# Optimization experiments

Measured on AMD Instinct MI355X. Metric: run time of the kernel, lower is better.

## Reference

```python
import jax, jax.numpy as jnp
import numpy as np

N, M, D = 16384, 1024, 1024


def setup_inputs() -> dict:
    key = jax.random.key(0)
    kq, kp = jax.random.split(key)
    query = jax.random.normal(kq, (N, D), dtype=jnp.float32)
    proto = jax.random.normal(kp, (M, D), dtype=jnp.float32)
    return {"query": query, "proto": proto}


def reference(query, proto):
    # Pairwise squared euclidean: ||q||^2 - 2 q.p + ||p||^2  (same math as
    # the expand+pow+sum in compute_euclidean, but without the [N,M,D] blowup).
    q2 = jnp.sum(query * query, axis=-1, keepdims=True)          # [N,1]
    p2 = jnp.sum(proto * proto, axis=-1)                          # [M]
    qp = jnp.einsum('nd,md->nm', query, proto)                    # [N,M]
    dists = q2 - 2.0 * qp + p2[None, :]                           # [N,M]
    # Original applies F.softmax(-dists, dim=1) (named log_p_y but is softmax).
    return jax.nn.softmax(-dists, axis=1)
```

## Files before the change

kernel.cpp:

```cpp
#include <hip/hip_runtime.h>
#include <stdint.h>

#define N_Q 16384
#define M_P 1024
#define D_K 1024

typedef __attribute__((ext_vector_type(8))) __bf16 bf16x8;
typedef __attribute__((ext_vector_type(4))) float floatx4;
typedef __attribute__((ext_vector_type(4))) unsigned int uint4v;

#define AS1 __attribute__((address_space(1)))
#define AS3 __attribute__((address_space(3)))

__device__ __forceinline__ unsigned short f2bf(float f) {
    unsigned int u = __float_as_uint(f);
    u += 0x7fffu + ((u >> 16) & 1u);
    return (unsigned short)(u >> 16);
}
__device__ __forceinline__ float bf2f(unsigned short h) {
    return __uint_as_float(((unsigned int)h) << 16);
}

__device__ __forceinline__ void split_chunk(floatx4 f0, floatx4 f1,
                                            uint4v* hi, uint4v* lo) {
    float e[8] = {f0.x, f0.y, f0.z, f0.w, f1.x, f1.y, f1.z, f1.w};
    unsigned int hb[4], lb[4];
#pragma unroll
    for (int p = 0; p < 4; ++p) {
        unsigned int u0 = __float_as_uint(e[2 * p]);
        unsigned int u1 = __float_as_uint(e[2 * p + 1]);
        hb[p] = __builtin_amdgcn_perm(u1, u0, 0x07060302);
        float l0 = e[2 * p]     - __uint_as_float(u0 & 0xffff0000u);
        float l1 = e[2 * p + 1] - __uint_as_float(u1 & 0xffff0000u);
        lb[p] = __builtin_amdgcn_perm(__float_as_uint(l1), __float_as_uint(l0),
                                      0x07060302);
    }
    uint4v h = {hb[0], hb[1], hb[2], hb[3]};
    uint4v l = {lb[0], lb[1], lb[2], lb[3]};
    *hi = h;
    *lo = l;
}

__global__ __launch_bounds__(256) void convert_proto_kernel(
    const float* __restrict__ proto, unsigned short* __restrict__ ph,
    unsigned short* __restrict__ pl, float* __restrict__ p2) {
    __shared__ float sred[4];
    int m = blockIdx.x;
    int t = threadIdx.x;
    size_t base4 = (size_t)m * (D_K / 4) + t;
    float4 v = ((const float4*)proto)[base4];
    ushort4 h, l;
    h.x = f2bf(v.x); l.x = f2bf(v.x - bf2f(h.x));
    h.y = f2bf(v.y); l.y = f2bf(v.y - bf2f(h.y));
    h.z = f2bf(v.z); l.z = f2bf(v.z - bf2f(h.z));
    h.w = f2bf(v.w); l.w = f2bf(v.w - bf2f(h.w));
    ((ushort4*)ph)[base4] = h;
    ((ushort4*)pl)[base4] = l;
    float sq = v.x * v.x + v.y * v.y + v.z * v.z + v.w * v.w;
#pragma unroll
    for (int off = 1; off < 64; off <<= 1) sq += __shfl_xor(sq, off);
    if ((t & 63) == 0) sred[t >> 6] = sq;
    __syncthreads();
    if (t == 0) p2[m] = sred[0] + sred[1] + sred[2] + sred[3];
}

__global__ __launch_bounds__(512, 2) void gemm_logits_kernel(
    const float* __restrict__ query,
    const unsigned short* __restrict__ ph, const unsigned short* __restrict__ pl,
    const float* __restrict__ p2, float* __restrict__ out) {
    __shared__ unsigned short sAh[2][16 * 512];
    __shared__ unsigned short sAl[2][16 * 512];
    __shared__ unsigned short sBh[2][16 * 512];
    __shared__ unsigned short sBl[2][16 * 512];

    const int tid = threadIdx.x;
    const int wave = tid >> 6;
    const int lane = tid & 63;
    const int wr = wave >> 2;
    const int wc = wave & 3;

    const int b = blockIdx.x;
    const int v = (b & 7) * 32 + (b >> 3);
    const int colt = v >> 6;
    const int rowt = v & 63;
    const int row0 = rowt * 256;
    const int col0 = colt * 256;

    const int rlB = lane >> 2;
    const int cioB = (lane & 3) ^ ((lane >> 3) & 3);
    const int halfB = wave >> 2;
    const int sgB = wave & 3;
    const unsigned short* gB = (halfB ? pl : ph)
        + (size_t)(col0 + sgB * 64 + rlB) * D_K + cioB * 8;

    const int rlA = lane >> 2;
    const int cA = lane & 3;
    const float* gA = query + (size_t)(row0 + wave * 32 + rlA) * D_K + cA * 8;
    const int wroff = (4 * rlA + (cA ^ ((rlA >> 1) & 3))) * 8;

    const int rsel = lane & 15;
    const int kq = lane >> 4;
    const int fragoff = (4 * rsel + (kq ^ ((rsel >> 1) & 3))) * 8;

    floatx4 zero = {0.0f, 0.0f, 0.0f, 0.0f};
    floatx4 acc[8][4];
#pragma unroll
    for (int i = 0; i < 8; ++i)
#pragma unroll
        for (int j = 0; j < 4; ++j) acc[i][j] = zero;

    floatx4 f0[2], f1[2];
    bf16x8 bh[4], bl[4];
    bf16x8 ah[2], al[2];

    auto issueA = [&](int kb) {
#pragma unroll
        for (int s = 0; s < 2; ++s) {
            const float* p = gA + (size_t)(s * 16) * D_K + kb;
            f0[s] = *(const floatx4*)p;
            f1[s] = *(const floatx4*)(p + 4);
        }
    };
    auto issueB = [&](int kb, int nxt) {
        unsigned short* dstB = (halfB ? sBl[nxt] : sBh[nxt]) + sgB * 4 * 512;
#pragma unroll
        for (int s = 0; s < 4; ++s)
            __builtin_amdgcn_global_load_lds(
                (const AS1 unsigned int*)(const void*)(gB + (size_t)(s * 16) * D_K + kb),
                (AS3 unsigned int*)(void*)(dstB + s * 512), 16, 0, 0);
    };
    auto writeA = [&](int nxt, int s) {
        uint4v hi, lo;
        split_chunk(f0[s], f1[s], &hi, &lo);
        const int off = (wave * 2 + s) * 512 + wroff;
        *(uint4v*)(sAh[nxt] + off) = hi;
        *(uint4v*)(sAl[nxt] + off) = lo;
    };
    auto ldBfrag = [&](int cur) {
#pragma unroll
        for (int j = 0; j < 4; ++j) {
            const int boff = (wc * 4 + j) * 512 + fragoff;
            bh[j] = *(const bf16x8*)(sBh[cur] + boff);
            bl[j] = *(const bf16x8*)(sBl[cur] + boff);
        }
    };
    auto ldAfrag = [&](int cur, int i0) {
#pragma unroll
        for (int t = 0; t < 2; ++t) {
            const int aoff = (wr * 8 + i0 + t) * 512 + fragoff;
            ah[t] = *(const bf16x8*)(sAh[cur] + aoff);
            al[t] = *(const bf16x8*)(sAl[cur] + aoff);
        }
    };
    auto mfma2 = [&](int i0) {
#pragma unroll
        for (int j = 0; j < 4; ++j)
#pragma unroll
            for (int t = 0; t < 2; ++t) {
                acc[i0 + t][j] = __builtin_amdgcn_mfma_f32_16x16x32_bf16(ah[t], bh[j], acc[i0 + t][j], 0, 0, 0);
                acc[i0 + t][j] = __builtin_amdgcn_mfma_f32_16x16x32_bf16(ah[t], bl[j], acc[i0 + t][j], 0, 0, 0);
                acc[i0 + t][j] = __builtin_amdgcn_mfma_f32_16x16x32_bf16(al[t], bh[j], acc[i0 + t][j], 0, 0, 0);
            }
    };

    auto stepf = [&](int kbn, int cur, int nxt, bool pf) {
        if (pf) { issueA(kbn); issueB(kbn, nxt); }
        ldBfrag(cur);
        ldAfrag(cur, 0);
        __builtin_amdgcn_s_barrier();
        __builtin_amdgcn_s_setprio(1); mfma2(0); __builtin_amdgcn_s_setprio(0);
        __builtin_amdgcn_s_barrier();
        ldAfrag(cur, 2);
        __builtin_amdgcn_s_barrier();
        __builtin_amdgcn_s_setprio(1); mfma2(2); __builtin_amdgcn_s_setprio(0);
        __builtin_amdgcn_s_barrier();
        ldAfrag(cur, 4);
        if (pf) writeA(nxt, 0);
        __builtin_amdgcn_s_barrier();
        __builtin_amdgcn_s_setprio(1); mfma2(4); __builtin_amdgcn_s_setprio(0);
        __builtin_amdgcn_s_barrier();
        ldAfrag(cur, 6);
        if (pf) writeA(nxt, 1);
        __syncthreads();
        __builtin_amdgcn_s_setprio(1); mfma2(6); __builtin_amdgcn_s_setprio(0);
    };

    issueA(0);
    issueB(0, 0);
    writeA(0, 0);
    writeA(0, 1);
    __syncthreads();

    for (int kt = 0; kt < 30; kt += 2) {
        stepf((kt + 1) * 32, 0, 1, true);
        stepf((kt + 2) * 32, 1, 0, true);
    }
    stepf(31 * 32, 0, 1, true);
    stepf(0, 1, 0, false);

#pragma unroll
    for (int j = 0; j < 4; ++j) {
        const int gc = col0 + wc * 64 + j * 16 + rsel;
        const float p2v = p2[gc];
#pragma unroll
        for (int i = 0; i < 8; ++i) {
            const int gr = row0 + wr * 128 + i * 16 + kq * 4;
#pragma unroll
            for (int r = 0; r < 4; ++r) {
                out[(size_t)(gr + r) * M_P + gc] = 2.0f * acc[i][j][r] - p2v;
            }
        }
    }
}

__global__ __launch_bounds__(256) void naive_logits_kernel(
    const float* __restrict__ query, const float* __restrict__ proto,
    float* __restrict__ out) {
    __shared__ float qs[D_K];
    int n = blockIdx.x;
    int t = threadIdx.x;
    ((float4*)qs)[t] = ((const float4*)(query + (size_t)n * D_K))[t];
    __syncthreads();
    float acc[4] = {0.f, 0.f, 0.f, 0.f};
    float pp[4] = {0.f, 0.f, 0.f, 0.f};
    for (int d = 0; d < D_K; d += 4) {
        float4 qv = *(const float4*)(qs + d);
#pragma unroll
        for (int j = 0; j < 4; ++j) {
            const float4 pv = *(const float4*)(proto + (size_t)(t + 256 * j) * D_K + d);
            acc[j] += qv.x * pv.x + qv.y * pv.y + qv.z * pv.z + qv.w * pv.w;
            pp[j] += pv.x * pv.x + pv.y * pv.y + pv.z * pv.z + pv.w * pv.w;
        }
    }
#pragma unroll
    for (int j = 0; j < 4; ++j)
        out[(size_t)n * M_P + t + 256 * j] = 2.0f * acc[j] - pp[j];
}

__global__ __launch_bounds__(256) void softmax_kernel(float* __restrict__ out) {
    const int lane = threadIdx.x & 63;
    int n = blockIdx.x * 4 + (threadIdx.x >> 6);
    for (int it = 0; it < 2; ++it, n += 8192) {
        float* row = out + (size_t)n * M_P;
        floatx4 v[4];
#pragma unroll
        for (int k = 0; k < 4; ++k)
            v[k] = *((const floatx4*)row + k * 64 + lane);
        float mx = fmaxf(fmaxf(v[0].x, v[0].y), fmaxf(v[0].z, v[0].w));
#pragma unroll
        for (int k = 1; k < 4; ++k)
            mx = fmaxf(mx, fmaxf(fmaxf(v[k].x, v[k].y), fmaxf(v[k].z, v[k].w)));
#pragma unroll
        for (int off = 1; off < 64; off <<= 1) mx = fmaxf(mx, __shfl_xor(mx, off));
        float s = 0.0f;
#pragma unroll
        for (int k = 0; k < 4; ++k) {
            v[k].x = __expf(v[k].x - mx);
            v[k].y = __expf(v[k].y - mx);
            v[k].z = __expf(v[k].z - mx);
            v[k].w = __expf(v[k].w - mx);
            s += v[k].x + v[k].y + v[k].z + v[k].w;
        }
#pragma unroll
        for (int off = 1; off < 64; off <<= 1) s += __shfl_xor(s, off);
        const float inv = 1.0f / s;
#pragma unroll
        for (int k = 0; k < 4; ++k) {
            floatx4 o;
            o.x = v[k].x * inv; o.y = v[k].y * inv;
            o.z = v[k].z * inv; o.w = v[k].w * inv;
            __builtin_nontemporal_store(o, (floatx4*)row + k * 64 + lane);
        }
    }
}

extern "C" void kernel_launch(void* const* d_in, const int* in_sizes, int n_in,
                              void* d_out, int out_size, void* d_ws, size_t ws_size,
                              hipStream_t stream) {
    const float* query = (const float*)d_in[0];
    const float* proto = (const float*)d_in[1];
    float* out = (float*)d_out;

    const size_t pElems = (size_t)M_P * D_K;
    const size_t needed = pElems * 2 * 2 + M_P * 4;

    if (ws_size >= needed) {
        unsigned short* ph = (unsigned short*)d_ws;
        unsigned short* pl = ph + pElems;
        float* p2 = (float*)(pl + pElems);

        convert_proto_kernel<<<M_P, 256, 0, stream>>>(proto, ph, pl, p2);
        gemm_logits_kernel<<<(N_Q / 256) * (M_P / 256), 512, 0, stream>>>(
            query, ph, pl, p2, out);
    } else {
        naive_logits_kernel<<<N_Q, 256, 0, stream>>>(query, proto, out);
    }
    softmax_kernel<<<2048, 256, 0, stream>>>(out);
}
```

Baseline: 206.6 us.

## Prefetch query tile one step further ahead with explicit waitcnt scheduling

The query (A) global loads are issued one k-step earlier, so the register-held fp32 data for step k+2 is in flight while step k computes, and both A-chunk writes to LDS move to the middle phase. Manual s_waitcnt lgkmcnt/vmcnt plus sched_barrier replace __syncthreads, so the wait is only on the B async LDS loads and the A loads stay outstanding. The A pointer is cast to global address space so the compiler emits global rather than flat loads. This adds register pressure and relies on exact vmcnt counts, which must match the number of outstanding loads.

```diff
diff --git a/kernel.cpp b/kernel.cpp
--- a/kernel.cpp
+++ b/kernel.cpp
@@ -95,7 +95,8 @@
 
     const int rlA = lane >> 2;
     const int cA = lane & 3;
-    const float* gA = query + (size_t)(row0 + wave * 32 + rlA) * D_K + cA * 8;
+    const AS1 float* gA = (const AS1 float*)query
+        + (size_t)(row0 + wave * 32 + rlA) * D_K + cA * 8;
     const int wroff = (4 * rlA + (cA ^ ((rlA >> 1) & 3))) * 8;
 
     const int rsel = lane & 15;
@@ -116,9 +117,9 @@
     auto issueA = [&](int kb) {
 #pragma unroll
         for (int s = 0; s < 2; ++s) {
-            const float* p = gA + (size_t)(s * 16) * D_K + kb;
-            f0[s] = *(const floatx4*)p;
-            f1[s] = *(const floatx4*)(p + 4);
+            const AS1 float* p = gA + (size_t)(s * 16) * D_K + kb;
+            f0[s] = *(const AS1 floatx4*)p;
+            f1[s] = *(const AS1 floatx4*)(p + 4);
         }
     };
     auto issueB = [&](int kb, int nxt) {
@@ -163,40 +164,56 @@
             }
     };
 
-    auto stepf = [&](int kbn, int cur, int nxt, bool pf) {
-        if (pf) { issueA(kbn); issueB(kbn, nxt); }
+#define PHASE_MFMA(i0)                                          \
+    __builtin_amdgcn_s_barrier();                               \
+    asm volatile("s_waitcnt lgkmcnt(0)" ::: "memory");          \
+    __builtin_amdgcn_sched_barrier(0);                          \
+    __builtin_amdgcn_s_setprio(1);                              \
+    mfma2(i0);                                                  \
+    __builtin_amdgcn_s_setprio(0);                              \
+    __builtin_amdgcn_s_barrier();
+
+    auto stepf = [&](int kbnB, int kbnA, int cur, int nxt, bool pfB, bool pfA) {
+        if (pfB) issueB(kbnB, nxt);
         ldBfrag(cur);
         ldAfrag(cur, 0);
+        PHASE_MFMA(0)
+        ldAfrag(cur, 2);
+        PHASE_MFMA(2)
+        ldAfrag(cur, 4);
+        if (pfB) { writeA(nxt, 0); writeA(nxt, 1); }
+        PHASE_MFMA(4)
+        ldAfrag(cur, 6);
+        if (pfA) issueA(kbnA);
+        asm volatile("s_waitcnt lgkmcnt(0)" ::: "memory");
+        if (pfB) {
+            if (pfA) asm volatile("s_waitcnt vmcnt(4)" ::: "memory");
+            else     asm volatile("s_waitcnt vmcnt(0)" ::: "memory");
+        }
         __builtin_amdgcn_s_barrier();
-        __builtin_amdgcn_s_setprio(1); mfma2(0); __builtin_amdgcn_s_setprio(0);
-        __builtin_amdgcn_s_barrier();
-        ldAfrag(cur, 2);
-        __builtin_amdgcn_s_barrier();
-        __builtin_amdgcn_s_setprio(1); mfma2(2); __builtin_amdgcn_s_setprio(0);
-        __builtin_amdgcn_s_barrier();
-        ldAfrag(cur, 4);
-        if (pf) writeA(nxt, 0);
-        __builtin_amdgcn_s_barrier();
-        __builtin_amdgcn_s_setprio(1); mfma2(4); __builtin_amdgcn_s_setprio(0);
-        __builtin_amdgcn_s_barrier();
-        ldAfrag(cur, 6);
-        if (pf) writeA(nxt, 1);
-        __syncthreads();
-        __builtin_amdgcn_s_setprio(1); mfma2(6); __builtin_amdgcn_s_setprio(0);
+        __builtin_amdgcn_sched_barrier(0);
+        __builtin_amdgcn_s_setprio(1);
+        mfma2(6);
+        __builtin_amdgcn_s_setprio(0);
     };
 
     issueA(0);
     issueB(0, 0);
     writeA(0, 0);
     writeA(0, 1);
-    __syncthreads();
+    issueA(32);
+    asm volatile("s_waitcnt lgkmcnt(0)" ::: "memory");
+    asm volatile("s_waitcnt vmcnt(4)" ::: "memory");
+    __builtin_amdgcn_s_barrier();
 
     for (int kt = 0; kt < 30; kt += 2) {
-        stepf((kt + 1) * 32, 0, 1, true);
-        stepf((kt + 2) * 32, 1, 0, true);
-    }
-    stepf(31 * 32, 0, 1, true);
-    stepf(0, 1, 0, false);
+        stepf((kt + 1) * 32, (kt + 2) * 32, 0, 1, true, true);
+        stepf((kt + 2) * 32, (kt + 3) * 32, 1, 0, true, true);
+    }
+    stepf(31 * 32, 0, 0, 1, true, false);
+    stepf(0, 0, 1, 0, false, false);
+
+#undef PHASE_MFMA
 
 #pragma unroll
     for (int j = 0; j < 4; ++j) {
```

Measured after the change: 202.0 us. -2.2%, faster.
